# Performance work log

Hardware: AMD Instinct MI355X
Metric: run time of the kernel (lower is better)

Reference implementation:

```python
import jax, jax.numpy as jnp
import numpy as np

K_VAL = 250       # k_val
STEP_SIZE = 0.1   # step_size
TEMP = 1.0        # proposal_temp


def setup_inputs() -> dict:
    key = jax.random.key(0)
    k1, k2, k3, k4 = jax.random.split(key, 4)
    B, S, E, V = 4, 512, 64, 50257
    return {
        "gx": jax.random.normal(k1, (B, S, E), dtype=jnp.float32),
        "cur_bias": jax.random.normal(k2, (B, S, E), dtype=jnp.float32),
        "embed_weight": jax.random.normal(k3, (V, E), dtype=jnp.float32),
        "logits": jax.random.normal(k4, (B, S, V), dtype=jnp.float32),
    }


def _unfiltered_dist(gx, cur_bias, W, step_size):
    # embed-space proposal distribution (proposal_rep_space == 'embed')
    t1_1 = jnp.einsum("bse,ve->bsv", gx, W)                      # [B,S,V]
    t1_2 = jnp.einsum("bse,bse->bs", gx, cur_bias)[..., None]    # [B,S,1]
    t2_1 = jnp.sum(W * W, axis=-1)[None, None, :]                # [1,1,V]
    t2_2 = jnp.einsum("bse,ve->bsv", cur_bias, W)                # [B,S,V]
    t2_3 = jnp.sum(cur_bias * cur_bias, axis=-1)[..., None]      # [B,S,1]
    dist = 0.5 * (t1_1 - t1_2) + (t2_1 - 2.0 * t2_2 + t2_3) / step_size
    return -dist


def reference(gx, cur_bias, embed_weight, logits):
    # proposal logits over the full vocab
    unfiltered = _unfiltered_dist(gx, cur_bias, embed_weight, STEP_SIZE)  # [B,S,V]
    # candidate selection: top-k token ids by LM logits
    _, topk_ids = jax.lax.top_k(logits, K_VAL)                            # [B,S,K]
    # gather proposal logits at the candidate ids, temperature scale
    filtered = jnp.take_along_axis(unfiltered, topk_ids, axis=-1) / TEMP  # [B,S,K]
    return filtered, topk_ids
```

## Files before the change

kernel.cpp:

```cpp
#include <hip/hip_runtime.h>
#include <stdint.h>

#define BB 4
#define SS 512
#define EE 64
#define VV 50257
#define KK 250
#define NROWS (BB * SS)
#define CAP 1024
#define NB 1024

#define THRF 2.4f

typedef float float4n __attribute__((ext_vector_type(4)));
typedef unsigned long long u64;

__device__ __forceinline__ unsigned fkey(float f) {
    unsigned u = __float_as_uint(f);
    return (u & 0x80000000u) ? ~u : (u | 0x80000000u);
}

__device__ __forceinline__ unsigned binOf(unsigned key) {
    unsigned b = (key - 0xC0000000u) >> 14;
    return b > (NB - 1u) ? (NB - 1u) : b;
}

__global__ __launch_bounds__(256, 8)
void select_ids(const float* __restrict__ lg,
                float* __restrict__ out1)
{
    __shared__ u64 lbuf[CAP];
    __shared__ unsigned hist[NB];
    __shared__ unsigned offs[NB];
    __shared__ unsigned wtot[4];
    __shared__ unsigned lcnt, sTbin;

    const int row = blockIdx.x;
    const int tid = threadIdx.x;
    const float* rp = lg + (size_t)row * VV;

    for (int j = tid; j < NB; j += 256) hist[j] = 0u;
    if (tid == 0) lcnt = 0u;
    __syncthreads();

    const unsigned p  = (4u - ((unsigned)((size_t)row * VV) & 3u)) & 3u;
    const unsigned F  = (VV - p) >> 2;
    const unsigned tail0 = p + 4u * F;
    const float4n* rp4 = (const float4n*)(rp + p);

    auto emit = [&](float f, unsigned col) {
        if (f >= THRF) {
            unsigned q = atomicAdd(&lcnt, 1u);
            if (q < CAP) lbuf[q] = ((u64)fkey(f) << 32) | (unsigned)(~col);
        }
    };

    if (tid < (int)p) emit(rp[tid], tid);
    unsigned i = tid;
    for (; i + 768u < F; i += 1024u) {
        float4n a = __builtin_nontemporal_load(&rp4[i]);
        float4n b = __builtin_nontemporal_load(&rp4[i + 256u]);
        float4n c = __builtin_nontemporal_load(&rp4[i + 512u]);
        float4n d = __builtin_nontemporal_load(&rp4[i + 768u]);
        float t0 = fmaxf(fmaxf(a.x, a.y), a.z);
        float t1 = fmaxf(fmaxf(a.w, b.x), b.y);
        float t2 = fmaxf(fmaxf(b.z, b.w), c.x);
        float t3 = fmaxf(fmaxf(c.y, c.z), c.w);
        float t4 = fmaxf(fmaxf(d.x, d.y), d.z);
        float u0 = fmaxf(fmaxf(t0, t1), t2);
        float u1 = fmaxf(fmaxf(t3, t4), d.w);
        if (fmaxf(u0, u1) >= THRF) {
            unsigned c0 = p + 4u*i, c1 = p + 4u*(i+256u), c2 = p + 4u*(i+512u), c3 = p + 4u*(i+768u);
            emit(a.x, c0+0); emit(a.y, c0+1); emit(a.z, c0+2); emit(a.w, c0+3);
            emit(b.x, c1+0); emit(b.y, c1+1); emit(b.z, c1+2); emit(b.w, c1+3);
            emit(c.x, c2+0); emit(c.y, c2+1); emit(c.z, c2+2); emit(c.w, c2+3);
            emit(d.x, c3+0); emit(d.y, c3+1); emit(d.z, c3+2); emit(d.w, c3+3);
        }
    }
    for (; i < F; i += 256u) {
        float4n a = __builtin_nontemporal_load(&rp4[i]);
        if (fmaxf(fmaxf(a.x, a.y), fmaxf(a.z, a.w)) >= THRF) {
            unsigned c0 = p + 4u*i;
            emit(a.x, c0+0); emit(a.y, c0+1); emit(a.z, c0+2); emit(a.w, c0+3);
        }
    }
    for (unsigned t = tail0 + tid; t < VV; t += 256u) emit(rp[t], t);
    __syncthreads();

    unsigned n = lcnt;

    if (n >= KK && n <= CAP) {
        u64 myk[4]; unsigned myb[4];
        #pragma unroll
        for (int s = 0; s < 4; ++s) {
            unsigned j = (unsigned)tid + 256u * s;
            myk[s] = 0ull; myb[s] = 0u;
            if (j < n) {
                u64 c = lbuf[j]; myk[s] = c;
                unsigned b = binOf((unsigned)(c >> 32)); myb[s] = b;
                atomicAdd(&hist[b], 1u);
            }
        }
        __syncthreads();

        unsigned h0 = hist[tid*4+0], h1 = hist[tid*4+1], h2 = hist[tid*4+2], h3 = hist[tid*4+3];
        unsigned ls3 = 0, ls2 = h3, ls1 = h3 + h2, ls0 = h3 + h2 + h1;
        unsigned tot = ls0 + h0;
        const unsigned lane = (unsigned)tid & 63u, wv = (unsigned)tid >> 6;
        unsigned incl = tot;
        #pragma unroll
        for (unsigned d = 1; d < 64; d <<= 1) {
            unsigned v = __shfl_down(incl, d, 64);
            if (lane + d < 64u) incl += v;
        }
        if (lane == 0) wtot[wv] = incl;
        __syncthreads();
        unsigned above = 0;
        #pragma unroll
        for (int ww = 0; ww < 4; ++ww) if (ww > (int)wv) above += wtot[ww];
        const unsigned exclSuf = (incl - tot) + above;
        offs[tid*4+0] = exclSuf + ls0;
        offs[tid*4+1] = exclSuf + ls1;
        offs[tid*4+2] = exclSuf + ls2;
        offs[tid*4+3] = exclSuf + ls3;
        __syncthreads();

        u64* sorted = lbuf;
        #pragma unroll
        for (int s = 0; s < 4; ++s) {
            unsigned j = (unsigned)tid + 256u * s;
            if (j < n) {
                unsigned pos = atomicAdd(&offs[myb[s]], 1u);
                sorted[pos] = myk[s];
            }
        }
        __syncthreads();

        #pragma unroll
        for (int s = 0; s < 4; ++s) {
            unsigned j = (unsigned)tid + 256u * s;
            if (j < n) {
                unsigned b = myb[s], cntb = hist[b], base = offs[b] - cntb;
                u64 k = myk[s];
                unsigned r = base;
                for (unsigned t2 = base; t2 < base + cntb; ++t2)
                    r += (sorted[t2] > k) ? 1u : 0u;
                if (r < KK) out1[(size_t)row * KK + r] = (float)(~(unsigned)k);
            }
        }
        return;
    }

    {
        unsigned* csum = offs;
        for (int j = tid; j < NB; j += 256) hist[j] = 0u;
        if (tid == 0) lcnt = 0u;
        __syncthreads();

        if (tid < (int)p) atomicAdd(&hist[fkey(rp[tid]) >> 22], 1u);
        for (unsigned j = tid; j < F; j += 256u) {
            float4n v = rp4[j];
            atomicAdd(&hist[fkey(v.x) >> 22], 1u); atomicAdd(&hist[fkey(v.y) >> 22], 1u);
            atomicAdd(&hist[fkey(v.z) >> 22], 1u); atomicAdd(&hist[fkey(v.w) >> 22], 1u);
        }
        for (unsigned t = tail0 + tid; t < VV; t += 256u) atomicAdd(&hist[fkey(rp[t]) >> 22], 1u);
        __syncthreads();

        csum[tid] = hist[tid*4] + hist[tid*4+1] + hist[tid*4+2] + hist[tid*4+3];
        __syncthreads();
        {
            unsigned g = 0;
            for (int u2 = tid + 1; u2 < 256; ++u2) g += csum[u2];
            unsigned cs = csum[tid];
            if (g < KK && g + cs >= KK) {
                unsigned cum = g;
                #pragma unroll
                for (int b2 = 3; b2 >= 0; --b2) {
                    unsigned c2 = hist[tid*4 + b2];
                    if (cum + c2 >= KK) { sTbin = (unsigned)(tid*4 + b2); break; }
                    cum += c2;
                }
            }
        }
        __syncthreads();
        const unsigned keyT = sTbin << 22;
        __syncthreads();

        auto emit2 = [&](float f, unsigned col) {
            unsigned k = fkey(f);
            if (k >= keyT) {
                unsigned q = atomicAdd(&lcnt, 1u);
                if (q < CAP) lbuf[q] = ((u64)k << 32) | (unsigned)(~col);
            }
        };
        if (tid < (int)p) emit2(rp[tid], tid);
        for (unsigned j = tid; j < F; j += 256u) {
            float4n v = rp4[j];
            unsigned ia = p + 4u*j;
            emit2(v.x, ia+0); emit2(v.y, ia+1); emit2(v.z, ia+2); emit2(v.w, ia+3);
        }
        for (unsigned t = tail0 + tid; t < VV; t += 256u) emit2(rp[t], t);
        __syncthreads();
        unsigned nf = lcnt; if (nf > CAP) nf = CAP;
        const unsigned P4 = (nf + 3u) & ~3u;
        for (unsigned j = nf + tid; j < P4; j += 256u) lbuf[j] = 0ull;
        __syncthreads();

        u64 k0 = ((unsigned)tid < nf)        ? lbuf[tid]        : 0ull;
        u64 k1 = ((unsigned)tid + 256u < nf) ? lbuf[tid + 256u] : 0ull;
        u64 k2 = ((unsigned)tid + 512u < nf) ? lbuf[tid + 512u] : 0ull;
        u64 k3 = ((unsigned)tid + 768u < nf) ? lbuf[tid + 768u] : 0ull;
        unsigned r0 = 0, r1 = 0, r2 = 0, r3 = 0;
        for (unsigned j = 0; j < P4; j += 4) {
            u64 a = lbuf[j], b = lbuf[j+1], c = lbuf[j+2], d = lbuf[j+3];
            r0 += (a > k0) + (b > k0) + (c > k0) + (d > k0);
            r1 += (a > k1) + (b > k1) + (c > k1) + (d > k1);
            r2 += (a > k2) + (b > k2) + (c > k2) + (d > k2);
            r3 += (a > k3) + (b > k3) + (c > k3) + (d > k3);
        }
        if ((unsigned)tid < nf        && r0 < KK) out1[(size_t)row * KK + r0] = (float)(~(unsigned)k0);
        if ((unsigned)tid + 256u < nf && r1 < KK) out1[(size_t)row * KK + r1] = (float)(~(unsigned)k1);
        if ((unsigned)tid + 512u < nf && r2 < KK) out1[(size_t)row * KK + r2] = (float)(~(unsigned)k2);
        if ((unsigned)tid + 768u < nf && r3 < KK) out1[(size_t)row * KK + r3] = (float)(~(unsigned)k3);
    }
}

__global__ __launch_bounds__(256)
void epilogue_kernel(const float* __restrict__ gx,
                     const float* __restrict__ cb,
                     const float* __restrict__ W,
                     const float* __restrict__ ids,
                     float* __restrict__ out0)
{
    __shared__ float u_s[EE];
    __shared__ float sCrow;
    const int row = blockIdx.x;
    const int tid = threadIdx.x;

    if (tid < EE) {
        float a = gx[(size_t)row * EE + tid];
        float b = cb[(size_t)row * EE + tid];
        u_s[tid] = 0.5f * a - 20.0f * b;
        float p1 = a * b, p2 = b * b;
        #pragma unroll
        for (int d = 32; d > 0; d >>= 1) {
            p1 += __shfl_xor(p1, d, 64);
            p2 += __shfl_xor(p2, d, 64);
        }
        if (tid == 0) sCrow = 0.5f * p1 - 10.0f * p2;
    }
    __syncthreads();

    const int grp = tid >> 4;
    const int l16 = tid & 15;
    const float4 u4 = *(const float4*)(u_s + 4 * l16);

    for (int k = grp; k < KK; k += 16) {
        unsigned v = (unsigned)ids[(size_t)row * KK + k];
        float4 w = *(const float4*)(W + (size_t)v * EE + 4 * l16);
        float acc = u4.x * w.x + u4.y * w.y + u4.z * w.z + u4.w * w.w
                  + 10.0f * (w.x * w.x + w.y * w.y + w.z * w.z + w.w * w.w);
        #pragma unroll
        for (int d = 8; d >= 1; d >>= 1) acc += __shfl_xor(acc, d, 16);
        if (l16 == 0) out0[(size_t)row * KK + k] = sCrow - acc;
    }
}

extern "C" void kernel_launch(void* const* d_in, const int* in_sizes, int n_in,
                              void* d_out, int out_size, void* d_ws, size_t ws_size,
                              hipStream_t stream) {
    const float* gx = (const float*)d_in[0];
    const float* cb = (const float*)d_in[1];
    const float* W  = (const float*)d_in[2];
    const float* lg = (const float*)d_in[3];
    float* out0 = (float*)d_out;
    float* out1 = out0 + (size_t)BB * SS * KK;

    hipLaunchKernelGGL(select_ids, dim3(NROWS), dim3(256), 0, stream, lg, out1);
    hipLaunchKernelGGL(epilogue_kernel, dim3(NROWS), dim3(256), 0, stream,
                       gx, cb, W, out1, out0);
}
```

Measured before the change: 98.53 us.

## Split streaming filter from selection and fuse selection with gather epilogue

The logits-streaming pass becomes a lean kernel that only collects threshold candidates into a global workspace, dropping its histogram and offset shared arrays. This lowers LDS use and should raise occupancy for the bandwidth-bound scan. The bin-sort ranking and the fallback path move into a second kernel, which also computes the embedding dot products from top ids held in shared memory instead of re-reading the id output. The cost is an extra global write and read of candidates, and the fallback path may have to rescan the logits in the second kernel.

```diff
diff --git a/kernel.cpp b/kernel.cpp
--- a/kernel.cpp
+++ b/kernel.cpp
@@ -26,20 +26,17 @@
 }
 
 __global__ __launch_bounds__(256, 8)
-void select_ids(const float* __restrict__ lg,
-                float* __restrict__ out1)
+void stream_kernel(const float* __restrict__ lg,
+                   u64* __restrict__ cand,
+                   unsigned* __restrict__ cnt)
 {
     __shared__ u64 lbuf[CAP];
-    __shared__ unsigned hist[NB];
-    __shared__ unsigned offs[NB];
-    __shared__ unsigned wtot[4];
-    __shared__ unsigned lcnt, sTbin;
+    __shared__ unsigned lcnt;
 
     const int row = blockIdx.x;
     const int tid = threadIdx.x;
     const float* rp = lg + (size_t)row * VV;
 
-    for (int j = tid; j < NB; j += 256) hist[j] = 0u;
     if (tid == 0) lcnt = 0u;
     __syncthreads();
 
@@ -87,7 +84,53 @@
     for (unsigned t = tail0 + tid; t < VV; t += 256u) emit(rp[t], t);
     __syncthreads();
 
-    unsigned n = lcnt;
+    const unsigned n = lcnt;
+    const unsigned m = n > CAP ? CAP : n;
+    for (unsigned j = tid; j < m; j += 256u)
+        cand[(size_t)row * CAP + j] = lbuf[j];
+    if (tid == 0) cnt[row] = n;
+}
+
+__global__ __launch_bounds__(256)
+void finish_kernel(const float* __restrict__ gx,
+                   const float* __restrict__ cb,
+                   const float* __restrict__ W,
+                   const float* __restrict__ lg,
+                   const u64* __restrict__ cand,
+                   const unsigned* __restrict__ cnt,
+                   float* __restrict__ out0,
+                   float* __restrict__ out1)
+{
+    __shared__ u64 sorted[CAP];
+    __shared__ unsigned hist[NB];
+    __shared__ unsigned offs[NB];
+    __shared__ unsigned top_ids[256];
+    __shared__ float u_s[EE];
+    __shared__ float sCrow;
+    __shared__ unsigned wtot[4];
+    __shared__ unsigned lcnt, sTbin;
+
+    const int row = blockIdx.x;
+    const int tid = threadIdx.x;
+    const float* rp = lg + (size_t)row * VV;
+
+    if (tid < 64) {
+        float a = gx[(size_t)row * EE + tid];
+        float b = cb[(size_t)row * EE + tid];
+        u_s[tid] = 0.5f * a - 20.0f * b;
+        float p1 = a * b, p2 = b * b;
+        #pragma unroll
+        for (int d = 32; d > 0; d >>= 1) {
+            p1 += __shfl_xor(p1, d, 64);
+            p2 += __shfl_xor(p2, d, 64);
+        }
+        if (tid == 0) sCrow = 0.5f * p1 - 10.0f * p2;
+    }
+    for (int j = tid; j < NB; j += 256) hist[j] = 0u;
+    if (tid == 0) lcnt = 0u;
+    __syncthreads();
+
+    const unsigned n = cnt[row];
 
     if (n >= KK && n <= CAP) {
         u64 myk[4]; unsigned myb[4];
@@ -96,7 +139,8 @@
             unsigned j = (unsigned)tid + 256u * s;
             myk[s] = 0ull; myb[s] = 0u;
             if (j < n) {
-                u64 c = lbuf[j]; myk[s] = c;
+                u64 c = cand[(size_t)row * CAP + j];
+                myk[s] = c;
                 unsigned b = binOf((unsigned)(c >> 32)); myb[s] = b;
                 atomicAdd(&hist[b], 1u);
             }
@@ -125,7 +169,6 @@
         offs[tid*4+3] = exclSuf + ls3;
         __syncthreads();
 
-        u64* sorted = lbuf;
         #pragma unroll
         for (int s = 0; s < 4; ++s) {
             unsigned j = (unsigned)tid + 256u * s;
@@ -145,17 +188,21 @@
                 unsigned r = base;
                 for (unsigned t2 = base; t2 < base + cntb; ++t2)
                     r += (sorted[t2] > k) ? 1u : 0u;
-                if (r < KK) out1[(size_t)row * KK + r] = (float)(~(unsigned)k);
-            }
-        }
-        return;
-    }
-
-    {
+                if (r < KK) {
+                    unsigned v = ~((unsigned)k);
+                    top_ids[r] = v;
+                    out1[(size_t)row * KK + r] = (float)v;
+                }
+            }
+        }
+        __syncthreads();
+    } else {
+        const unsigned p  = (4u - ((unsigned)((size_t)row * VV) & 3u)) & 3u;
+        const unsigned F  = (VV - p) >> 2;
+        const unsigned tail0 = p + 4u * F;
+        const float4n* rp4 = (const float4n*)(rp + p);
         unsigned* csum = offs;
-        for (int j = tid; j < NB; j += 256) hist[j] = 0u;
-        if (tid == 0) lcnt = 0u;
-        __syncthreads();
+        u64* lbuf = sorted;
 
         if (tid < (int)p) atomicAdd(&hist[fkey(rp[tid]) >> 22], 1u);
         for (unsigned j = tid; j < F; j += 256u) {
@@ -218,45 +265,26 @@
             r2 += (a > k2) + (b > k2) + (c > k2) + (d > k2);
             r3 += (a > k3) + (b > k3) + (c > k3) + (d > k3);
         }
-        if ((unsigned)tid < nf        && r0 < KK) out1[(size_t)row * KK + r0] = (float)(~(unsigned)k0);
-        if ((unsigned)tid + 256u < nf && r1 < KK) out1[(size_t)row * KK + r1] = (float)(~(unsigned)k1);
-        if ((unsigned)tid + 512u < nf && r2 < KK) out1[(size_t)row * KK + r2] = (float)(~(unsigned)k2);
-        if ((unsigned)tid + 768u < nf && r3 < KK) out1[(size_t)row * KK + r3] = (float)(~(unsigned)k3);
-    }
-}
-
-__global__ __launch_bounds__(256)
-void epilogue_kernel(const float* __restrict__ gx,
-                     const float* __restrict__ cb,
-                     const float* __restrict__ W,
-                     const float* __restrict__ ids,
-                     float* __restrict__ out0)
-{
-    __shared__ float u_s[EE];
-    __shared__ float sCrow;
-    const int row = blockIdx.x;
-    const int tid = threadIdx.x;
-
-    if (tid < EE) {
-        float a = gx[(size_t)row * EE + tid];
-        float b = cb[(size_t)row * EE + tid];
-        u_s[tid] = 0.5f * a - 20.0f * b;
-        float p1 = a * b, p2 = b * b;
-        #pragma unroll
-        for (int d = 32; d > 0; d >>= 1) {
-            p1 += __shfl_xor(p1, d, 64);
-            p2 += __shfl_xor(p2, d, 64);
-        }
-        if (tid == 0) sCrow = 0.5f * p1 - 10.0f * p2;
-    }
-    __syncthreads();
+        auto rec = [&](u64 k, unsigned r, bool act) {
+            if (act && r < KK) {
+                unsigned v = ~((unsigned)k);
+                top_ids[r] = v;
+                out1[(size_t)row * KK + r] = (float)v;
+            }
+        };
+        rec(k0, r0, (unsigned)tid < nf);
+        rec(k1, r1, (unsigned)tid + 256u < nf);
+        rec(k2, r2, (unsigned)tid + 512u < nf);
+        rec(k3, r3, (unsigned)tid + 768u < nf);
+        __syncthreads();
+    }
 
     const int grp = tid >> 4;
     const int l16 = tid & 15;
     const float4 u4 = *(const float4*)(u_s + 4 * l16);
 
     for (int k = grp; k < KK; k += 16) {
-        unsigned v = (unsigned)ids[(size_t)row * KK + k];
+        unsigned v = top_ids[k];
         float4 w = *(const float4*)(W + (size_t)v * EE + 4 * l16);
         float acc = u4.x * w.x + u4.y * w.y + u4.z * w.z + u4.w * w.w
                   + 10.0f * (w.x * w.x + w.y * w.y + w.z * w.z + w.w * w.w);
@@ -276,7 +304,11 @@
     float* out0 = (float*)d_out;
     float* out1 = out0 + (size_t)BB * SS * KK;
 
-    hipLaunchKernelGGL(select_ids, dim3(NROWS), dim3(256), 0, stream, lg, out1);
-    hipLaunchKernelGGL(epilogue_kernel, dim3(NROWS), dim3(256), 0, stream,
-                       gx, cb, W, out1, out0);
-}
+    unsigned* cnt = (unsigned*)d_ws;
+    u64* cand = (u64*)((char*)d_ws + 32768);
+
+    hipLaunchKernelGGL(stream_kernel, dim3(NROWS), dim3(256), 0, stream,
+                       lg, cand, cnt);
+    hipLaunchKernelGGL(finish_kernel, dim3(NROWS), dim3(256), 0, stream,
+                       gx, cb, W, lg, cand, cnt, out0, out1);
+}
```

New measurement: 98.74 us. No clear change (+0.2%).
